# Kernel tuning notes

Hardware: AMD Instinct MI355X
Metric: run time of the kernel (lower is better)

Reference implementation:

```python
import jax, jax.numpy as jnp
import numpy as np

DIM_IN = 1024
DIM_QK = 1024
DIM_V = 1024


def setup_inputs() -> dict:
    key = jax.random.key(0)
    ks = jax.random.split(key, 8)
    s = DIM_IN ** -0.5
    return {
        "x": jax.random.normal(ks[0], (16, 2048, DIM_IN), dtype=jnp.float32),
        "encoder_output": jax.random.normal(ks[1], (16, 2048, DIM_IN), dtype=jnp.float32),
        "W_q": jax.random.normal(ks[2], (DIM_IN, DIM_QK), dtype=jnp.float32) * s,
        "b_q": jnp.zeros((DIM_QK,), dtype=jnp.float32),
        "W_k": jax.random.normal(ks[3], (DIM_IN, DIM_QK), dtype=jnp.float32) * s,
        "b_k": jnp.zeros((DIM_QK,), dtype=jnp.float32),
        "W_v": jax.random.normal(ks[4], (DIM_IN, DIM_V), dtype=jnp.float32) * s,
        "b_v": jnp.zeros((DIM_V,), dtype=jnp.float32),
    }


def reference(x, encoder_output, W_q, b_q, W_k, b_k, W_v, b_v):
    # Q: [B, Lq, Dqk]; K, V: [B, Lk, Dqk/Dv]
    Q = x @ W_q + b_q
    K = encoder_output @ W_k + b_k
    V = encoder_output @ W_v + b_v
    # attn_scores: [B, Lq, Lk], scaled by 1/sqrt(Dqk)
    scores = jnp.einsum("bqd,bkd->bqk", Q, K) * (K.shape[-1] ** -0.5)
    weights = jax.nn.softmax(scores, axis=-1)
    H = jnp.einsum("bqk,bkv->bqv", weights, V)  # [B, Lq, Dv]
    return H
```

## Files before the change

### kernel.cpp

```cpp
#include <hip/hip_runtime.h>

typedef _Float16 f16;
typedef __attribute__((ext_vector_type(4))) _Float16 f16x4;
typedef __attribute__((ext_vector_type(8))) _Float16 f16x8;
typedef __attribute__((ext_vector_type(4))) float f32x4;

#define MFMA16(a, b, c) __builtin_amdgcn_mfma_f32_16x16x32_f16(a, b, c, 0, 0, 0)

__device__ __forceinline__ void gll16(const void* g, void* l) {
    __builtin_amdgcn_global_load_lds(
        (const __attribute__((address_space(1))) unsigned int*)g,
        (__attribute__((address_space(3))) unsigned int*)l, 16, 0, 0);
}

#define BAR() __builtin_amdgcn_s_barrier()
#define VMC(n)  asm volatile("s_waitcnt vmcnt(" #n ")" ::: "memory")

__global__ __launch_bounds__(256) void prep_all(
    const float* __restrict__ x, const float* __restrict__ enc,
    const float* __restrict__ Wq, const float* __restrict__ Wk,
    const float* __restrict__ Wv,
    f16* __restrict__ Xh, f16* __restrict__ Eh, f16* __restrict__ Wt)
{
    const int bid = blockIdx.x;
    if (bid < 32768) {
        const float* in = (bid < 16384) ? x : enc;
        f16* out = (bid < 16384) ? Xh : Eh;
        const int b = bid & 16383;
        const size_t i = ((size_t)b * 256 + threadIdx.x) * 8;
        float4 a = *(const float4*)(in + i);
        float4 c = *(const float4*)(in + i + 4);
        f16x8 o;
        o[0] = (f16)a.x; o[1] = (f16)a.y; o[2] = (f16)a.z; o[3] = (f16)a.w;
        o[4] = (f16)c.x; o[5] = (f16)c.y; o[6] = (f16)c.z; o[7] = (f16)c.w;
        *(f16x8*)(out + i) = o;
        return;
    }
    __shared__ float tile[32][33];
    const int id2 = bid - 32768;
    const int w = id2 >> 10;
    const int r = id2 & 1023;
    const int n0 = (r & 31) * 32, k0 = (r >> 5) * 32;
    const float* W = w == 0 ? Wq : (w == 1 ? Wk : Wv);
    f16* dst = Wt + (size_t)w * 1024 * 1024;
    const int tx = threadIdx.x & 31, ty = threadIdx.x >> 5;
#pragma unroll
    for (int i = 0; i < 4; i++)
        tile[ty + i * 8][tx] = W[(size_t)(k0 + ty + i * 8) * 1024 + n0 + tx];
    __syncthreads();
#pragma unroll
    for (int i = 0; i < 4; i++)
        dst[(size_t)(n0 + ty + i * 8) * 1024 + k0 + tx] = (f16)tile[tx][ty + i * 8];
}

template <int KD, int EPI>
__global__ __launch_bounds__(512, 2) void gemm8(
    const f16* __restrict__ Ab, const f16* __restrict__ Ab2,
    const f16* __restrict__ Bb,
    const float* __restrict__ b0, const float* __restrict__ b1,
    const float* __restrict__ b2, float scale,
    void* __restrict__ C0, void* __restrict__ C1, void* __restrict__ C2,
    float* __restrict__ aux,
    size_t strA, size_t strB, size_t strC, int ldc, int nbx, int nby)
{
    __shared__ f16 shA[2 * 256 * 64];
    __shared__ f16 shB[2 * 256 * 64];

    int id = blockIdx.x;
    {
        const int chunk = (int)gridDim.x >> 3;
        id = (id & 7) * chunk + (id >> 3);
    }
    int bx, by, z;
    bool isQ = false;
    if constexpr (EPI == 4) {
        z = 0;
        isQ = (id < 512);
        if (isQ) { by = id & 3; bx = id >> 2; }
        else     { const int id2 = id - 512; by = id2 & 7; bx = id2 >> 3; }
    } else {
        by = id % nby;
        const int r2 = id / nby;
        bx = r2 % nbx;
        z  = r2 / nbx;
    }
    const int bm = bx * 256, bn = by * 256;

    const f16* A;
    const f16* B;
    if constexpr (EPI == 4) {
        A = isQ ? Ab : Ab2;
        B = Bb + (isQ ? (size_t)0 : (size_t)1024 * 1024);
    } else {
        A = Ab + (size_t)z * strA;
        B = Bb + (size_t)z * strB;
    }

    const int t = threadIdx.x, lane = t & 63, wid = t >> 6;
    const int wr = wid >> 2, wc = wid & 3;
    const int fr = lane & 15, kb = (lane >> 4) * 16;
    const int sw = (fr & 7) << 4;

    const int lsr = lane >> 3;
    const int lsc = ((lane & 7) * 16) ^ (lsr << 4);
    const int a_  = wid * 8;
    const int bq_ = (wid >> 2) * 64 + (wid & 3) * 8;
    const f16* aT0 = A + (size_t)(bm + lsr) * KD + (lsc >> 1) + (size_t)a_ * KD;
    const f16* bT0 = B + (size_t)(bn + lsr) * KD + (lsc >> 1) + (size_t)bq_ * KD;

    const char* Ab_ = (const char*)shA;
    const char* Bb_ = (const char*)shB;
    const int aoffk0 = (wr * 128 + fr) * 128 + (kb ^ sw);
    const int aoffk1 = (wr * 128 + fr) * 128 + ((64 | kb) ^ sw);
    const int boffk0 = (wc * 64 + fr) * 128 + (kb ^ sw);
    const int boffk1 = (wc * 64 + fr) * 128 + ((64 | kb) ^ sw);

#define STG_A0(d, kt) do {                                                    \
        const f16* As_ = aT0 + (size_t)(kt) * 64;                             \
        gll16(As_,                      shA + (d) * 16384 + (a_)*64);         \
        gll16(As_ + (size_t)128 * KD,   shA + (d) * 16384 + (128 + a_)*64); } while (0)
#define STG_A1(d, kt) do {                                                    \
        const f16* As_ = aT0 + (size_t)(kt) * 64;                             \
        gll16(As_ + (size_t)64 * KD,    shA + (d) * 16384 + (64 + a_)*64);    \
        gll16(As_ + (size_t)192 * KD,   shA + (d) * 16384 + (192 + a_)*64); } while (0)
#define STG_B0(d, kt) do {                                                    \
        const f16* Bs_ = bT0 + (size_t)(kt) * 64;                             \
        gll16(Bs_,                      shB + (d) * 16384 + (bq_)*64);        \
        gll16(Bs_ + (size_t)128 * KD,   shB + (d) * 16384 + (128 + bq_)*64); } while (0)
#define STG_B1(d, kt) do {                                                    \
        const f16* Bs_ = bT0 + (size_t)(kt) * 64;                             \
        gll16(Bs_ + (size_t)32 * KD,    shB + (d) * 16384 + (32 + bq_)*64);   \
        gll16(Bs_ + (size_t)160 * KD,   shB + (d) * 16384 + (160 + bq_)*64); } while (0)

    f16x8 af[2][2][4];
    f16x8 bf[2][2][2];
    f32x4 acc[8][4] = {};

#define LDA_(d, mh)                                                           \
    _Pragma("unroll") for (int i_ = 0; i_ < 4; ++i_) {                        \
        af[mh][0][i_] = *(const f16x8*)(Ab_ + (d) * 32768 + aoffk0 +          \
                                        ((mh) * 64 + i_ * 16) * 128);         \
        af[mh][1][i_] = *(const f16x8*)(Ab_ + (d) * 32768 + aoffk1 +          \
                                        ((mh) * 64 + i_ * 16) * 128);         \
    }
#define LDB_(d, nh)                                                           \
    _Pragma("unroll") for (int j_ = 0; j_ < 2; ++j_) {                        \
        bf[nh][0][j_] = *(const f16x8*)(Bb_ + (d) * 32768 + boffk0 +          \
                                        ((nh) * 32 + j_ * 16) * 128);         \
        bf[nh][1][j_] = *(const f16x8*)(Bb_ + (d) * 32768 + boffk1 +          \
                                        ((nh) * 32 + j_ * 16) * 128);         \
    }

#define MM(mh, nh)                                                            \
    _Pragma("unroll") for (int kk_ = 0; kk_ < 2; ++kk_)                       \
    _Pragma("unroll") for (int i_ = 0; i_ < 4; ++i_)                          \
    _Pragma("unroll") for (int j_ = 0; j_ < 2; ++j_)                          \
        acc[(mh) * 4 + i_][(nh) * 2 + j_] =                                   \
            MFMA16(af[mh][kk_][i_], bf[nh][kk_][j_],                          \
                   acc[(mh) * 4 + i_][(nh) * 2 + j_]);

#define TILE_FULL(d, kt)                                                      \
    do {                                                                      \
        LDA_(d, 0); LDB_(d, 0); LDB_(d, 1);                                   \
        STG_A0((d) ^ 1, (kt) + 1); STG_B0((d) ^ 1, (kt) + 1);                 \
        STG_B1((d) ^ 1, (kt) + 1);                                            \
        VMC(6);                                                               \
        BAR(); MM(0, 0); MM(0, 1); BAR();                                     \
        LDA_(d, 1);                                                           \
        STG_A1((d) ^ 1, (kt) + 1);                                            \
        VMC(2);                                                               \
        BAR(); MM(1, 1); MM(1, 0); BAR();                                     \
    } while (0)

#define TILE_TAIL(d)                                                          \
    do {                                                                      \
        LDA_(d, 0); LDB_(d, 0); LDB_(d, 1);                                   \
        VMC(0);                                                               \
        BAR(); MM(0, 0); MM(0, 1); BAR();                                     \
        LDA_(d, 1);                                                           \
        BAR(); MM(1, 1); MM(1, 0); BAR();                                     \
    } while (0)

    constexpr int NT = KD / 64;

    STG_A0(0, 0); STG_B0(0, 0); STG_B1(0, 0); STG_A1(0, 0);
    VMC(2);
    BAR();

    for (int ti = 0; ti < NT - 2; ti += 2) {
        TILE_FULL(0, ti);
        TILE_FULL(1, ti + 1);
    }
    TILE_FULL(0, NT - 2);
    TILE_TAIL(1);

    const int fc = lane & 15, rq = (lane >> 4) * 4;

    if constexpr (EPI == 2) {
        BAR();
        float* part = (float*)shA;
        f16* Sp = (f16*)C0 + (size_t)z * strC;
#pragma unroll
        for (int mi = 0; mi < 8; ++mi)
#pragma unroll
            for (int r = 0; r < 4; ++r) {
                const int rl = wr * 128 + mi * 16 + rq + r;
                float ps = 0.f;
#pragma unroll
                for (int nj = 0; nj < 4; ++nj) {
                    const int col = bn + wc * 64 + nj * 16 + fc;
                    f16 eh = (f16)__expf(acc[mi][nj][r]);
                    ps += (float)eh;
                    Sp[(size_t)(bm + rl) * ldc + col] = eh;
                }
#pragma unroll
                for (int o = 1; o < 16; o <<= 1) ps += __shfl_xor(ps, o);
                if (fc == 0) part[rl * 4 + wc] = ps;
            }
        BAR();
        if (t < 256) {
            const float4 p4 = *(const float4*)(part + t * 4);
            aux[((size_t)z * 2048 + bm + t) * 8 + by] = p4.x + p4.y + p4.z + p4.w;
        }
        return;
    }

    if constexpr (EPI == 5) {
        float invr[8][4];
#pragma unroll
        for (int mi = 0; mi < 8; ++mi)
#pragma unroll
            for (int r = 0; r < 4; ++r) {
                const int row = bm + wr * 128 + mi * 16 + rq + r;
                const float4* p = (const float4*)(aux + ((size_t)z * 2048 + row) * 8);
                const float4 a = p[0], b = p[1];
                invr[mi][r] = 1.0f / (a.x + a.y + a.z + a.w + b.x + b.y + b.z + b.w);
            }
#pragma unroll
        for (int nj = 0; nj < 4; ++nj) {
            const int col = bn + wc * 64 + nj * 16 + fc;
#pragma unroll
            for (int mi = 0; mi < 8; ++mi)
#pragma unroll
                for (int r = 0; r < 4; ++r) {
                    const int row = bm + wr * 128 + mi * 16 + rq + r;
                    ((float*)C0 + (size_t)z * strC)[(size_t)row * ldc + col] =
                        acc[mi][nj][r] * invr[mi][r];
                }
        }
        return;
    }

    if constexpr (EPI == 4) {
#pragma unroll
        for (int nj = 0; nj < 4; ++nj) {
            const int col = bn + wc * 64 + nj * 16 + fc;
            if (isQ) {
                const float bv_ = b0[col];
#pragma unroll
                for (int mi = 0; mi < 8; ++mi)
#pragma unroll
                    for (int r = 0; r < 4; ++r) {
                        const int row = bm + wr * 128 + mi * 16 + rq + r;
                        ((f16*)C0)[(size_t)row * 1024 + col] =
                            (f16)((acc[mi][nj][r] + bv_) * scale);
                    }
            } else {
                const float bv_ = (col < 1024) ? b1[col] : b2[col - 1024];
#pragma unroll
                for (int mi = 0; mi < 8; ++mi) {
                    if (col >= 1024) {
                        const int rowb = bm + wr * 128 + mi * 16 + rq;
                        f16x4 q;
#pragma unroll
                        for (int r = 0; r < 4; ++r) q[r] = (f16)(acc[mi][nj][r] + bv_);
                        f16* Cp = (f16*)C2 + (size_t)(rowb >> 11) * 2048 * 1024 +
                                  (size_t)(col - 1024) * 2048;
                        *(f16x4*)&Cp[rowb & 2047] = q;
                    } else {
#pragma unroll
                        for (int r = 0; r < 4; ++r) {
                            const int row = bm + wr * 128 + mi * 16 + rq + r;
                            ((f16*)C1)[(size_t)row * 1024 + col] =
                                (f16)(acc[mi][nj][r] + bv_);
                        }
                    }
                }
            }
        }
        return;
    }
#undef STG_A0
#undef STG_A1
#undef STG_B0
#undef STG_B1
#undef LDA_
#undef LDB_
#undef MM
#undef TILE_FULL
#undef TILE_TAIL
}

extern "C" void kernel_launch(void* const* d_in, const int* in_sizes, int n_in,
                              void* d_out, int out_size, void* d_ws, size_t ws_size,
                              hipStream_t stream)
{
    const float* x   = (const float*)d_in[0];
    const float* enc = (const float*)d_in[1];
    const float* Wq  = (const float*)d_in[2];
    const float* bq  = (const float*)d_in[3];
    const float* Wk  = (const float*)d_in[4];
    const float* bk  = (const float*)d_in[5];
    const float* Wv  = (const float*)d_in[6];
    const float* bv  = (const float*)d_in[7];

    const size_t TOK = (size_t)16 * 2048;
    f16* Qh = (f16*)d_ws;
    f16* Kh = Qh + TOK * 1024;
    f16* Vt = Kh + TOK * 1024;
    f16* Wt = Vt + TOK * 1024;
    f16* S  = Wt + (size_t)3 * 1024 * 1024;
    f16* Xh = S;
    f16* Eh = S + TOK * 1024;
    float* Ppart = (float*)Wt;

    prep_all<<<35840, 256, 0, stream>>>(x, enc, Wq, Wk, Wv, Xh, Eh, Wt);

    gemm8<1024, 4><<<1536, 512, 0, stream>>>(
        Xh, Eh, Wt, bq, bk, bv, 0.03125f, Qh, Kh, Vt, nullptr,
        0, 0, 0, 1024, 128, 0);

    gemm8<1024, 2><<<1024, 512, 0, stream>>>(
        Qh, nullptr, Kh, nullptr, nullptr, nullptr, 1.0f, S, nullptr, nullptr,
        Ppart,
        (size_t)2048 * 1024, (size_t)2048 * 1024, (size_t)2048 * 2048, 2048, 8, 8);

    gemm8<2048, 5><<<512, 512, 0, stream>>>(
        S, nullptr, Vt, nullptr, nullptr, nullptr, 1.0f, d_out, nullptr, nullptr,
        Ppart,
        (size_t)2048 * 2048, (size_t)1024 * 2048, (size_t)2048 * 1024, 1024, 8, 4);
}
```

Baseline: 625.1 us.

## Fuse fp32-to-fp16 activation conversion into the projection GEMM

Removes the standalone pass that converted x and encoder_output to fp16, and instead has a new projection kernel load fp32 activation tiles into registers, convert them, and store fp16 into LDS. Weight transposition becomes its own small kernel. This avoids writing and re-reading the full fp16 activation copies. In exchange, each GEMM block reads twice as many bytes of A from global memory, uses more registers, and runs a simpler pipeline with a block-wide barrier per tile.

```diff
diff --git a/kernel.cpp b/kernel.cpp
--- a/kernel.cpp
+++ b/kernel.cpp
@@ -16,34 +16,15 @@
 #define BAR() __builtin_amdgcn_s_barrier()
 #define VMC(n)  asm volatile("s_waitcnt vmcnt(" #n ")" ::: "memory")
 
-__global__ __launch_bounds__(256) void prep_all(
-    const float* __restrict__ x, const float* __restrict__ enc,
+__global__ __launch_bounds__(256) void prep_weights(
     const float* __restrict__ Wq, const float* __restrict__ Wk,
-    const float* __restrict__ Wv,
-    f16* __restrict__ Xh, f16* __restrict__ Eh, f16* __restrict__ Wt)
+    const float* __restrict__ Wv, f16* __restrict__ Wt)
 {
-    const int bid = blockIdx.x;
-    if (bid < 32768) {
-        const float* in = (bid < 16384) ? x : enc;
-        f16* out = (bid < 16384) ? Xh : Eh;
-        const int b = bid & 16383;
-        const size_t i = ((size_t)b * 256 + threadIdx.x) * 8;
-        float4 a = *(const float4*)(in + i);
-        float4 c = *(const float4*)(in + i + 4);
-        f16x8 o;
-        o[0] = (f16)a.x; o[1] = (f16)a.y; o[2] = (f16)a.z; o[3] = (f16)a.w;
-        o[4] = (f16)c.x; o[5] = (f16)c.y; o[6] = (f16)c.z; o[7] = (f16)c.w;
-        *(f16x8*)(out + i) = o;
-        return;
-    }
     __shared__ float tile[32][33];
-    const int id2 = bid - 32768;
-    const int w = id2 >> 10;
-    const int r = id2 & 1023;
-    const int n0 = (r & 31) * 32, k0 = (r >> 5) * 32;
-    const float* W = w == 0 ? Wq : (w == 1 ? Wk : Wv);
-    f16* dst = Wt + (size_t)w * 1024 * 1024;
+    const float* W = blockIdx.z == 0 ? Wq : (blockIdx.z == 1 ? Wk : Wv);
+    f16* dst = Wt + (size_t)blockIdx.z * 1024 * 1024;
     const int tx = threadIdx.x & 31, ty = threadIdx.x >> 5;
+    const int n0 = blockIdx.x * 32, k0 = blockIdx.y * 32;
 #pragma unroll
     for (int i = 0; i < 4; i++)
         tile[ty + i * 8][tx] = W[(size_t)(k0 + ty + i * 8) * 1024 + n0 + tx];
@@ -53,14 +34,181 @@
         dst[(size_t)(n0 + ty + i * 8) * 1024 + k0 + tx] = (f16)tile[tx][ty + i * 8];
 }
 
+template <int KD>
+__global__ __launch_bounds__(512, 2) void proj32(
+    const float* __restrict__ xA, const float* __restrict__ eA,
+    const f16* __restrict__ Wt,
+    const float* __restrict__ bq, const float* __restrict__ bk,
+    const float* __restrict__ bv, float scale,
+    f16* __restrict__ Qh, f16* __restrict__ Kh, f16* __restrict__ VtOut)
+{
+    __shared__ f16 shA[2 * 256 * 64];
+    __shared__ f16 shB[2 * 256 * 64];
+
+    int id = blockIdx.x;
+    {
+        const int chunk = (int)gridDim.x >> 3;
+        id = (id & 7) * chunk + (id >> 3);
+    }
+    const bool isQ = (id < 512);
+    int bx, by;
+    if (isQ) { by = id & 3; bx = id >> 2; }
+    else     { const int id2 = id - 512; by = id2 & 7; bx = id2 >> 3; }
+    const int bm = bx * 256, bn = by * 256;
+
+    const float* A = isQ ? xA : eA;
+    const f16* B = Wt + (isQ ? (size_t)0 : (size_t)1024 * 1024);
+
+    const int t = threadIdx.x, lane = t & 63, wid = t >> 6;
+    const int wr = wid >> 2, wc = wid & 3;
+    const int fr = lane & 15, kb = (lane >> 4) * 16;
+    const int sw = (fr & 7) << 4;
+
+    const int lsr = lane >> 3;
+    const int lsc = ((lane & 7) * 16) ^ (lsr << 4);
+    const int bq_ = (wid >> 2) * 64 + (wid & 3) * 8;
+    const f16* bT0 = B + (size_t)(bn + lsr) * KD + (lsc >> 1) + (size_t)bq_ * KD;
+
+    const int ar_ = t >> 1;
+    const int ah_ = (t & 1) * 64;
+    const int asw = (ar_ & 7) << 4;
+    const float* aRow = A + (size_t)(bm + ar_) * KD;
+    int aelem[4];
+#pragma unroll
+    for (int c = 0; c < 4; ++c) aelem[c] = ((ah_ + c * 16) ^ asw) >> 1;
+
+    const char* Ab_ = (const char*)shA;
+    const char* Bb_ = (const char*)shB;
+    const int aoffk0 = (wr * 128 + fr) * 128 + (kb ^ sw);
+    const int aoffk1 = (wr * 128 + fr) * 128 + ((64 | kb) ^ sw);
+    const int boffk0 = (wc * 64 + fr) * 128 + (kb ^ sw);
+    const int boffk1 = (wc * 64 + fr) * 128 + ((64 | kb) ^ sw);
+
+#define STG_B0(d, kt) do {                                                    \
+        const f16* Bs_ = bT0 + (size_t)(kt) * 64;                             \
+        gll16(Bs_,                      shB + (d) * 16384 + (bq_)*64);        \
+        gll16(Bs_ + (size_t)128 * KD,   shB + (d) * 16384 + (128 + bq_)*64); } while (0)
+#define STG_B1(d, kt) do {                                                    \
+        const f16* Bs_ = bT0 + (size_t)(kt) * 64;                             \
+        gll16(Bs_ + (size_t)32 * KD,    shB + (d) * 16384 + (32 + bq_)*64);   \
+        gll16(Bs_ + (size_t)160 * KD,   shB + (d) * 16384 + (160 + bq_)*64); } while (0)
+
+    float4 av[8];
+#define LOADA(kt)                                                             \
+    _Pragma("unroll") for (int c = 0; c < 4; ++c) {                           \
+        av[2 * c]     = *(const float4*)(aRow + (size_t)(kt) * 64 + aelem[c]);\
+        av[2 * c + 1] = *(const float4*)(aRow + (size_t)(kt) * 64 + aelem[c] + 4); }
+#define WRITEA(d)                                                             \
+    _Pragma("unroll") for (int c = 0; c < 4; ++c) {                           \
+        f16x8 o_;                                                             \
+        o_[0] = (f16)av[2*c].x;   o_[1] = (f16)av[2*c].y;                     \
+        o_[2] = (f16)av[2*c].z;   o_[3] = (f16)av[2*c].w;                     \
+        o_[4] = (f16)av[2*c+1].x; o_[5] = (f16)av[2*c+1].y;                   \
+        o_[6] = (f16)av[2*c+1].z; o_[7] = (f16)av[2*c+1].w;                   \
+        *(f16x8*)((char*)shA + (d) * 32768 + ar_ * 128 + ah_ + c * 16) = o_; }
+
+    f16x8 af[2][2][4];
+    f16x8 bf[2][2][2];
+    f32x4 acc[8][4] = {};
+
+#define LDA_(d, mh)                                                           \
+    _Pragma("unroll") for (int i_ = 0; i_ < 4; ++i_) {                        \
+        af[mh][0][i_] = *(const f16x8*)(Ab_ + (d) * 32768 + aoffk0 +          \
+                                        ((mh) * 64 + i_ * 16) * 128);         \
+        af[mh][1][i_] = *(const f16x8*)(Ab_ + (d) * 32768 + aoffk1 +          \
+                                        ((mh) * 64 + i_ * 16) * 128);         \
+    }
+#define LDB_(d, nh)                                                           \
+    _Pragma("unroll") for (int j_ = 0; j_ < 2; ++j_) {                        \
+        bf[nh][0][j_] = *(const f16x8*)(Bb_ + (d) * 32768 + boffk0 +          \
+                                        ((nh) * 32 + j_ * 16) * 128);         \
+        bf[nh][1][j_] = *(const f16x8*)(Bb_ + (d) * 32768 + boffk1 +          \
+                                        ((nh) * 32 + j_ * 16) * 128);         \
+    }
+#define MM(mh, nh)                                                            \
+    _Pragma("unroll") for (int kk_ = 0; kk_ < 2; ++kk_)                       \
+    _Pragma("unroll") for (int i_ = 0; i_ < 4; ++i_)                          \
+    _Pragma("unroll") for (int j_ = 0; j_ < 2; ++j_)                          \
+        acc[(mh) * 4 + i_][(nh) * 2 + j_] =                                   \
+            MFMA16(af[mh][kk_][i_], bf[nh][kk_][j_],                          \
+                   acc[(mh) * 4 + i_][(nh) * 2 + j_]);
+
+    constexpr int NT = KD / 64;
+
+#define PTILE(d, kt)                                                          \
+    do {                                                                      \
+        if ((kt) + 1 < NT) {                                                  \
+            LOADA((kt) + 1);                                                  \
+            STG_B0((d) ^ 1, (kt) + 1); STG_B1((d) ^ 1, (kt) + 1);             \
+        }                                                                     \
+        LDA_(d, 0); LDB_(d, 0); LDB_(d, 1);                                   \
+        MM(0, 0); MM(0, 1);                                                   \
+        LDA_(d, 1);                                                           \
+        MM(1, 1); MM(1, 0);                                                   \
+        if ((kt) + 1 < NT) WRITEA((d) ^ 1);                                   \
+        __syncthreads();                                                      \
+    } while (0)
+
+    LOADA(0);
+    STG_B0(0, 0); STG_B1(0, 0);
+    WRITEA(0);
+    __syncthreads();
+
+    for (int ti = 0; ti < NT; ti += 2) {
+        PTILE(0, ti);
+        PTILE(1, ti + 1);
+    }
+
+    const int fc = lane & 15, rq = (lane >> 4) * 4;
+#pragma unroll
+    for (int nj = 0; nj < 4; ++nj) {
+        const int col = bn + wc * 64 + nj * 16 + fc;
+        if (isQ) {
+            const float bv_ = bq[col];
+#pragma unroll
+            for (int mi = 0; mi < 8; ++mi)
+#pragma unroll
+                for (int r = 0; r < 4; ++r) {
+                    const int row = bm + wr * 128 + mi * 16 + rq + r;
+                    Qh[(size_t)row * 1024 + col] =
+                        (f16)((acc[mi][nj][r] + bv_) * scale);
+                }
+        } else {
+            const float bv_ = (col < 1024) ? bk[col] : bv[col - 1024];
+#pragma unroll
+            for (int mi = 0; mi < 8; ++mi) {
+                if (col >= 1024) {
+                    const int rowb = bm + wr * 128 + mi * 16 + rq;
+                    f16x4 q;
+#pragma unroll
+                    for (int r = 0; r < 4; ++r) q[r] = (f16)(acc[mi][nj][r] + bv_);
+                    f16* Cp = VtOut + (size_t)(rowb >> 11) * 2048 * 1024 +
+                              (size_t)(col - 1024) * 2048;
+                    *(f16x4*)&Cp[rowb & 2047] = q;
+                } else {
+#pragma unroll
+                    for (int r = 0; r < 4; ++r) {
+                        const int row = bm + wr * 128 + mi * 16 + rq + r;
+                        Kh[(size_t)row * 1024 + col] = (f16)(acc[mi][nj][r] + bv_);
+                    }
+                }
+            }
+        }
+    }
+#undef STG_B0
+#undef STG_B1
+#undef LOADA
+#undef WRITEA
+#undef LDA_
+#undef LDB_
+#undef MM
+#undef PTILE
+}
+
 template <int KD, int EPI>
 __global__ __launch_bounds__(512, 2) void gemm8(
-    const f16* __restrict__ Ab, const f16* __restrict__ Ab2,
-    const f16* __restrict__ Bb,
-    const float* __restrict__ b0, const float* __restrict__ b1,
-    const float* __restrict__ b2, float scale,
-    void* __restrict__ C0, void* __restrict__ C1, void* __restrict__ C2,
-    float* __restrict__ aux,
+    const f16* __restrict__ Ab, const f16* __restrict__ Bb,
+    void* __restrict__ C0, float* __restrict__ aux,
     size_t strA, size_t strB, size_t strC, int ldc, int nbx, int nby)
 {
     __shared__ f16 shA[2 * 256 * 64];
@@ -71,30 +219,14 @@
         const int chunk = (int)gridDim.x >> 3;
         id = (id & 7) * chunk + (id >> 3);
     }
-    int bx, by, z;
-    bool isQ = false;
-    if constexpr (EPI == 4) {
-        z = 0;
-        isQ = (id < 512);
-        if (isQ) { by = id & 3; bx = id >> 2; }
-        else     { const int id2 = id - 512; by = id2 & 7; bx = id2 >> 3; }
-    } else {
-        by = id % nby;
-        const int r2 = id / nby;
-        bx = r2 % nbx;
-        z  = r2 / nbx;
-    }
+    const int by = id % nby;
+    const int r2 = id / nby;
+    const int bx = r2 % nbx;
+    const int z  = r2 / nbx;
     const int bm = bx * 256, bn = by * 256;
 
-    const f16* A;
-    const f16* B;
-    if constexpr (EPI == 4) {
-        A = isQ ? Ab : Ab2;
-        B = Bb + (isQ ? (size_t)0 : (size_t)1024 * 1024);
-    } else {
-        A = Ab + (size_t)z * strA;
-        B = Bb + (size_t)z * strB;
-    }
+    const f16* A = Ab + (size_t)z * strA;
+    const f16* B = Bb + (size_t)z * strB;
 
     const int t = threadIdx.x, lane = t & 63, wid = t >> 6;
     const int wr = wid >> 2, wc = wid & 3;
@@ -150,7 +282,6 @@
         bf[nh][1][j_] = *(const f16x8*)(Bb_ + (d) * 32768 + boffk1 +          \
                                         ((nh) * 32 + j_ * 16) * 128);         \
     }
-
 #define MM(mh, nh)                                                            \
     _Pragma("unroll") for (int kk_ = 0; kk_ < 2; ++kk_)                       \
     _Pragma("unroll") for (int i_ = 0; i_ < 4; ++i_)                          \
@@ -250,46 +381,6 @@
         }
         return;
     }
-
-    if constexpr (EPI == 4) {
-#pragma unroll
-        for (int nj = 0; nj < 4; ++nj) {
-            const int col = bn + wc * 64 + nj * 16 + fc;
-            if (isQ) {
-                const float bv_ = b0[col];
-#pragma unroll
-                for (int mi = 0; mi < 8; ++mi)
-#pragma unroll
-                    for (int r = 0; r < 4; ++r) {
-                        const int row = bm + wr * 128 + mi * 16 + rq + r;
-                        ((f16*)C0)[(size_t)row * 1024 + col] =
-                            (f16)((acc[mi][nj][r] + bv_) * scale);
-                    }
-            } else {
-                const float bv_ = (col < 1024) ? b1[col] : b2[col - 1024];
-#pragma unroll
-                for (int mi = 0; mi < 8; ++mi) {
-                    if (col >= 1024) {
-                        const int rowb = bm + wr * 128 + mi * 16 + rq;
-                        f16x4 q;
-#pragma unroll
-                        for (int r = 0; r < 4; ++r) q[r] = (f16)(acc[mi][nj][r] + bv_);
-                        f16* Cp = (f16*)C2 + (size_t)(rowb >> 11) * 2048 * 1024 +
-                                  (size_t)(col - 1024) * 2048;
-                        *(f16x4*)&Cp[rowb & 2047] = q;
-                    } else {
-#pragma unroll
-                        for (int r = 0; r < 4; ++r) {
-                            const int row = bm + wr * 128 + mi * 16 + rq + r;
-                            ((f16*)C1)[(size_t)row * 1024 + col] =
-                                (f16)(acc[mi][nj][r] + bv_);
-                        }
-                    }
-                }
-            }
-        }
-        return;
-    }
 #undef STG_A0
 #undef STG_A1
 #undef STG_B0
@@ -320,23 +411,18 @@
     f16* Vt = Kh + TOK * 1024;
     f16* Wt = Vt + TOK * 1024;
     f16* S  = Wt + (size_t)3 * 1024 * 1024;
-    f16* Xh = S;
-    f16* Eh = S + TOK * 1024;
     float* Ppart = (float*)Wt;
 
-    prep_all<<<35840, 256, 0, stream>>>(x, enc, Wq, Wk, Wv, Xh, Eh, Wt);
-
-    gemm8<1024, 4><<<1536, 512, 0, stream>>>(
-        Xh, Eh, Wt, bq, bk, bv, 0.03125f, Qh, Kh, Vt, nullptr,
-        0, 0, 0, 1024, 128, 0);
+    prep_weights<<<dim3(32, 32, 3), 256, 0, stream>>>(Wq, Wk, Wv, Wt);
+
+    proj32<1024><<<1536, 512, 0, stream>>>(
+        x, enc, Wt, bq, bk, bv, 0.03125f, Qh, Kh, Vt);
 
     gemm8<1024, 2><<<1024, 512, 0, stream>>>(
-        Qh, nullptr, Kh, nullptr, nullptr, nullptr, 1.0f, S, nullptr, nullptr,
-        Ppart,
+        Qh, Kh, S, Ppart,
         (size_t)2048 * 1024, (size_t)2048 * 1024, (size_t)2048 * 2048, 2048, 8, 8);
 
     gemm8<2048, 5><<<512, 512, 0, stream>>>(
-        S, nullptr, Vt, nullptr, nullptr, nullptr, 1.0f, d_out, nullptr, nullptr,
-        Ppart,
+        S, Vt, d_out, Ppart,
         (size_t)2048 * 2048, (size_t)1024 * 2048, (size_t)2048 * 1024, 1024, 8, 4);
 }
```

Result: slower. 675.5 us (+8.1%).
